# Optimization experiments

Measured on AMD Instinct MI355X. Metric: run time of the kernel, lower is better.

Reference implementation:

```python
import jax, jax.numpy as jnp
import numpy as np

B, S, D, H = 4, 2048, 1024, 16
DH = D // H  # 64
EPS = 1e-5


def setup_inputs() -> dict:
    key = jax.random.key(0)
    ks = jax.random.split(key, 6)
    scale = 0.02
    return {
        "x": jax.random.normal(ks[0], (B, S, D), dtype=jnp.float32),
        "Wq": jax.random.normal(ks[1], (H, D, DH), dtype=jnp.float32) * scale,
        "Wk": jax.random.normal(ks[2], (H, D, DH), dtype=jnp.float32) * scale,
        "Wv": jax.random.normal(ks[3], (H, D, DH), dtype=jnp.float32) * scale,
        "Wo": jax.random.normal(ks[4], (D, D), dtype=jnp.float32) * scale,
        "bo": jnp.zeros((D,), dtype=jnp.float32),
        "gamma": jnp.ones((D,), dtype=jnp.float32),
        "beta": jnp.zeros((D,), dtype=jnp.float32),
    }


def reference(x, Wq, Wk, Wv, Wo, bo, gamma, beta):
    # Per-head projections, stacked across heads: [B,H,S,DH]
    q = jnp.einsum("bsd,hdk->bhsk", x, Wq)
    k = jnp.einsum("bsd,hdk->bhsk", x, Wk)
    v = jnp.einsum("bsd,hdk->bhsk", x, Wv)
    inv_scale = 1.0 / jnp.sqrt(jnp.float32(DH))  # key.size(-1) == head_dim
    scores = jnp.einsum("bhqk,bhsk->bhqs", q, k) * inv_scale  # [B,H,S,S]
    attn = jax.nn.softmax(scores, axis=-1)
    ctx = jnp.einsum("bhqs,bhsk->bhqk", attn, v)  # [B,H,S,DH]
    # concat heads -> [B,S,D]
    concat = jnp.transpose(ctx, (0, 2, 1, 3)).reshape(B, S, D)
    proj = concat @ Wo + bo  # fc_out (Wo stored as [in,out])
    added = proj + x  # residual add
    mu = jnp.mean(added, axis=-1, keepdims=True)
    var = jnp.mean(jnp.square(added - mu), axis=-1, keepdims=True)
    normed = (added - mu) * jax.lax.rsqrt(var + EPS)
    return normed * gamma + beta
```

## Files before the change

### kernel.cpp

```cpp
#include <hip/hip_runtime.h>
#include <hip/hip_bf16.h>
#include <stdint.h>

#define DEV __device__ __forceinline__

typedef short s16x8 __attribute__((ext_vector_type(8)));
typedef float f32x4 __attribute__((ext_vector_type(4)));
typedef int i32x4 __attribute__((ext_vector_type(4)));

DEV void async_load16(const void* g, void* l) {
  __builtin_amdgcn_global_load_lds((void __attribute__((address_space(1)))*)(g),
                                   (void __attribute__((address_space(3)))*)(l),
                                   16, 0, 0);
}

DEV unsigned pack_bf16x2(float a, float b) {
  __hip_bfloat162 h = __float22bfloat162_rn(make_float2(a, b));
  union { __hip_bfloat162 h2; unsigned u; } cv;
  cv.h2 = h;
  return cv.u;
}

__global__ __launch_bounds__(256) void cast_x_kernel(const float* __restrict__ in,
                                                     __hip_bfloat16* __restrict__ out, int n4) {
  int i = blockIdx.x * 256 + threadIdx.x;
  if (i >= n4) return;
  float4 v = ((const float4*)in)[i];
  alignas(8) __hip_bfloat16 t[4] = {__float2bfloat16(v.x), __float2bfloat16(v.y),
                                    __float2bfloat16(v.z), __float2bfloat16(v.w)};
  *(uint2*)(out + (size_t)i * 4) = *(const uint2*)t;
}

__global__ __launch_bounds__(256) void transpose_cast_kernel(const float* __restrict__ src,
                                                             __hip_bfloat16* __restrict__ dst,
                                                             int R, int C, float scale) {
  __shared__ float tile[64][65];
  const int r0 = blockIdx.x * 64, c0 = blockIdx.y * 64, bt = blockIdx.z;
  const int tc = threadIdx.x & 63, tr = threadIdx.x >> 6;
  const float* sp = src + (size_t)bt * R * C;
#pragma unroll
  for (int rr = 0; rr < 64; rr += 4)
    tile[tr + rr][tc] = sp[(size_t)(r0 + tr + rr) * C + c0 + tc];
  __syncthreads();
  __hip_bfloat16* dp = dst + (size_t)bt * R * C;
#pragma unroll
  for (int rr = 0; rr < 64; rr += 4) {
    int cc = tr + rr;
    dp[(size_t)(c0 + cc) * R + r0 + tc] = __float2bfloat16(tile[tc][cc] * scale);
  }
}

__global__ __launch_bounds__(256) void qkv_transpose_kernel(const float* __restrict__ Wq,
                                                            const float* __restrict__ Wk,
                                                            const float* __restrict__ Wv,
                                                            __hip_bfloat16* __restrict__ dst,
                                                            float qscale) {
  __shared__ float tile[64][65];
  const int z = blockIdx.z, which = z >> 4, bt = z & 15;
  const int r0 = blockIdx.x * 64;
  const int tc = threadIdx.x & 63, tr = threadIdx.x >> 6;
  const float* src = (which == 0) ? Wq : (which == 1) ? Wk : Wv;
  const float scale = (which == 0) ? qscale : 1.0f;
  const float* sp = src + (size_t)bt * 1024 * 64;
#pragma unroll
  for (int rr = 0; rr < 64; rr += 4)
    tile[tr + rr][tc] = sp[(size_t)(r0 + tr + rr) * 64 + tc];
  __syncthreads();
  __hip_bfloat16* dp = dst + (size_t)z * 1024 * 64;
#pragma unroll
  for (int rr = 0; rr < 64; rr += 4) {
    int cc = tr + rr;
    dp[(size_t)(cc)*1024 + r0 + tc] = __float2bfloat16(tile[tc][cc] * scale);
  }
}

template <int MODE>
__global__ __launch_bounds__(256) void gemm128(const __hip_bfloat16* __restrict__ A,
                                               const __hip_bfloat16* __restrict__ Bt,
                                               void* __restrict__ out0,
                                               void* __restrict__ out1,
                                               void* __restrict__ out2,
                                               const float* __restrict__ bias,
                                               const float* __restrict__ resid,
                                               int M, int N, int K) {
  __shared__ __hip_bfloat16 As[128 * 32];
  __shared__ __hip_bfloat16 Bs[128 * 32];
  const int tid = threadIdx.x;
  const int lane = tid & 63, w = tid >> 6;
  const int lr = lane & 15, lq = lane >> 4;
  const int wm = w >> 1, wn = w & 1;
  const int m0 = blockIdx.y * 128, n0 = blockIdx.x * 128;

  const f32x4 fz = {0.f, 0.f, 0.f, 0.f};
  f32x4 acc[4][4];
#pragma unroll
  for (int i = 0; i < 4; i++)
#pragma unroll
    for (int j = 0; j < 4; j++) acc[i][j] = fz;

  const int kiters = K >> 5;
  for (int kt = 0; kt < kiters; kt++) {
    __syncthreads();
#pragma unroll
    for (int r = 0; r < 2; r++) {
      const int c = r * 256 + tid;
      const int row = c >> 2, kc = c & 3;
      async_load16((const short*)A + (size_t)(m0 + row) * K + kt * 32 + kc * 8,
                   (char*)As + (r * 256 + (tid & 0xC0)) * 16);
      async_load16((const short*)Bt + (size_t)(n0 + row) * K + kt * 32 + kc * 8,
                   (char*)Bs + (r * 256 + (tid & 0xC0)) * 16);
    }
    __syncthreads();
    const short* Ap = (const short*)As;
    const short* Bp = (const short*)Bs;
    s16x8 av[4], bv[4];
#pragma unroll
    for (int i = 0; i < 4; i++)
      av[i] = *(const s16x8*)(Ap + (wm * 64 + i * 16 + lr) * 32 + lq * 8);
#pragma unroll
    for (int j = 0; j < 4; j++)
      bv[j] = *(const s16x8*)(Bp + (wn * 64 + j * 16 + lr) * 32 + lq * 8);
#pragma unroll
    for (int i = 0; i < 4; i++)
#pragma unroll
      for (int j = 0; j < 4; j++)
        acc[i][j] = __builtin_amdgcn_mfma_f32_16x16x32_bf16(av[i], bv[j], acc[i][j], 0, 0, 0);
  }

  if constexpr (MODE == 0) {
    if (n0 < 2048) {
      __hip_bfloat16* dst01 = (__hip_bfloat16*)((n0 < 1024) ? out0 : out1);
#pragma unroll
      for (int i = 0; i < 4; i++)
#pragma unroll
        for (int j = 0; j < 4; j++)
#pragma unroll
          for (int r = 0; r < 4; r++) {
            const int row = m0 + wm * 64 + i * 16 + lq * 4 + r;
            const int col = n0 + wn * 64 + j * 16 + lr;
            const int bb = row >> 11, s = row & 2047;
            const int colq = col & 1023;
            dst01[((((size_t)bb * 16 + (colq >> 6)) * 2048 + s) << 6) + (col & 63)] =
                __float2bfloat16(acc[i][j][r]);
          }
    } else {
#pragma unroll
      for (int i = 0; i < 4; i++)
#pragma unroll
        for (int j = 0; j < 4; j++) {
          const int row0 = m0 + wm * 64 + i * 16 + lq * 4;
          const int col = (n0 - 2048) + wn * 64 + j * 16 + lr;
          const int bb = row0 >> 11, s0 = row0 & 2047;
          alignas(8) __hip_bfloat16 t4[4] = {
              __float2bfloat16(acc[i][j][0]), __float2bfloat16(acc[i][j][1]),
              __float2bfloat16(acc[i][j][2]), __float2bfloat16(acc[i][j][3])};
          *(uint2*)((__hip_bfloat16*)out2 + (size_t)bb * 2097152 + (size_t)col * 2048 + s0) =
              *(const uint2*)t4;
        }
    }
  } else {
#pragma unroll
    for (int i = 0; i < 4; i++)
#pragma unroll
      for (int j = 0; j < 4; j++)
#pragma unroll
        for (int r = 0; r < 4; r++) {
          const int row = m0 + wm * 64 + i * 16 + lq * 4 + r;
          const int col = n0 + wn * 64 + j * 16 + lr;
          const size_t idx = (size_t)row * 1024 + col;
          ((float*)out0)[idx] = acc[i][j][r] + bias[col] + resid[idx];
        }
  }
}

__global__ __launch_bounds__(256, 4) void flash_kernel(const __hip_bfloat16* __restrict__ Qg,
                                                       const __hip_bfloat16* __restrict__ Kg,
                                                       const __hip_bfloat16* __restrict__ Vtg,
                                                       __hip_bfloat16* __restrict__ Og) {
  __shared__ alignas(16) char smem[32768];
  float* xch = (float*)smem;
  const int tid = threadIdx.x;
  const int lane = tid & 63, w = tid >> 6;
  const int lr = lane & 15, lq = lane >> 4;
  const int qp = w >> 1;
  const int kvh = w & 1;
  const int hb = blockIdx.x, qt = blockIdx.y;
  const int h = hb >> 2, b = hb & 3;
  const size_t bh = (size_t)b * 16 + h;
  const short* Qbase = (const short*)Qg + (bh * 2048 + (size_t)qt * 64) * 64;
  const short* Kbh = (const short*)Kg + bh * 2048 * 64;
  const short* Vbh = (const short*)Vtg + bh * 64 * 2048;

  const int rbase = (lr >> 2) * 8 + (lr & 3);
  const int gk = lr & 7;

  s16x8 qb[2][2];
#pragma unroll
  for (int ntl = 0; ntl < 2; ntl++)
#pragma unroll
    for (int ks = 0; ks < 2; ks++)
      qb[ntl][ks] =
          *(const s16x8*)(Qbase + ((qp * 2 + ntl) * 16 + lr) * 64 + ks * 32 + lq * 8);

  s16x8 vones;
#pragma unroll
  for (int e = 0; e < 8; e++) vones[e] = (short)0x3F80;

  const f32x4 fz = {0.f, 0.f, 0.f, 0.f};
  f32x4 o[2][4];
  f32x4 ol[2];
#pragma unroll
  for (int i = 0; i < 2; i++) {
    ol[i] = fz;
#pragma unroll
    for (int j = 0; j < 4; j++) o[i][j] = fz;
  }

  auto stage = [&](int sel, int kb) {
    char* Kl = smem + sel * 16384;
    char* Vl = Kl + 8192;
    const short* Ksrc = Kbh + kb * 64 * 64;
#pragma unroll
    for (int r = 0; r < 2; r++) {
      int c = r * 256 + tid;
      int row = c >> 3, ck = c & 7;
      int g = (row & 3) | (((row >> 3) & 1) << 2);
      async_load16(Ksrc + row * 64 + (ck ^ g) * 8, Kl + (r * 256 + (tid & 0xC0)) * 16);
    }
#pragma unroll
    for (int r = 0; r < 2; r++) {
      int c = r * 256 + tid;
      int row = c >> 3, ck = c & 7;
      async_load16(Vbh + (size_t)row * 2048 + kb * 64 + ((ck ^ (row & 7))) * 8,
                   Vl + (r * 256 + (tid & 0xC0)) * 16);
    }
  };

  stage(0, 0);
  __syncthreads();

  for (int kb = 0; kb < 32; kb++) {
    const int cur = kb & 1;
    if (kb + 1 < 32) stage(cur ^ 1, kb + 1);

    const short* Kp = (const short*)(smem + cur * 16384);
    const short* Vp = (const short*)(smem + cur * 16384 + 8192);

    union { i32x4 i; s16x8 s; } pa[2];
#pragma unroll
    for (int mt = 0; mt < 2; mt++) {
      const int kvrow = kvh * 32 + mt * 4 + rbase;
      s16x8 kf0 = *(const s16x8*)(Kp + kvrow * 64 + (((0 * 4 + lq) ^ gk)) * 8);
      s16x8 kf1 = *(const s16x8*)(Kp + kvrow * 64 + (((1 * 4 + lq) ^ gk)) * 8);
#pragma unroll
      for (int ntl = 0; ntl < 2; ntl++) {
        f32x4 st = fz;
        st = __builtin_amdgcn_mfma_f32_16x16x32_bf16(kf0, qb[ntl][0], st, 0, 0, 0);
        st = __builtin_amdgcn_mfma_f32_16x16x32_bf16(kf1, qb[ntl][1], st, 0, 0, 0);
        float e0 = __builtin_amdgcn_exp2f(st[0]);
        float e1 = __builtin_amdgcn_exp2f(st[1]);
        float e2 = __builtin_amdgcn_exp2f(st[2]);
        float e3 = __builtin_amdgcn_exp2f(st[3]);
        pa[ntl].i[mt * 2 + 0] = (int)pack_bf16x2(e0, e1);
        pa[ntl].i[mt * 2 + 1] = (int)pack_bf16x2(e2, e3);
      }
    }
    __builtin_amdgcn_s_setprio(1);
#pragma unroll
    for (int ntl = 0; ntl < 2; ntl++)
      ol[ntl] = __builtin_amdgcn_mfma_f32_16x16x32_bf16(pa[ntl].s, vones, ol[ntl], 0, 0, 0);
#pragma unroll
    for (int ndh = 0; ndh < 4; ndh++) {
      int vrow = ndh * 16 + lr;
      s16x8 vb = *(const s16x8*)(Vp + vrow * 64 + (((kvh * 4 + lq) ^ (vrow & 7))) * 8);
#pragma unroll
      for (int ntl = 0; ntl < 2; ntl++)
        o[ntl][ndh] =
            __builtin_amdgcn_mfma_f32_16x16x32_bf16(pa[ntl].s, vb, o[ntl][ndh], 0, 0, 0);
    }
    __builtin_amdgcn_s_setprio(0);

    __syncthreads();
  }

  float* slot = xch + w * 1280;
  if (kvh == 0) {
#pragma unroll
    for (int ndh = 0; ndh < 4; ndh++)
      *(f32x4*)(slot + ndh * 256 + lane * 4) = o[1][ndh];
    *(f32x4*)(slot + 1024 + lane * 4) = ol[1];
  } else {
#pragma unroll
    for (int ndh = 0; ndh < 4; ndh++)
      *(f32x4*)(slot + ndh * 256 + lane * 4) = o[0][ndh];
    *(f32x4*)(slot + 1024 + lane * 4) = ol[0];
  }
  __syncthreads();
  const float* ps = xch + (w ^ 1) * 1280;
  if (kvh == 0) {
#pragma unroll
    for (int ndh = 0; ndh < 4; ndh++)
      o[0][ndh] += *(const f32x4*)(ps + ndh * 256 + lane * 4);
    f32x4 lt = ol[0] + *(const f32x4*)(ps + 1024 + lane * 4);
#pragma unroll
    for (int r = 0; r < 4; r++) {
      float inv = __builtin_amdgcn_rcpf(lt[r]);
      int rowg = qt * 64 + w * 16 + lq * 4 + r;
#pragma unroll
      for (int ndh = 0; ndh < 4; ndh++)
        Og[((size_t)b * 2048 + rowg) * 1024 + h * 64 + ndh * 16 + lr] =
            __float2bfloat16(o[0][ndh][r] * inv);
    }
  } else {
#pragma unroll
    for (int ndh = 0; ndh < 4; ndh++)
      o[1][ndh] += *(const f32x4*)(ps + ndh * 256 + lane * 4);
    f32x4 lt = ol[1] + *(const f32x4*)(ps + 1024 + lane * 4);
#pragma unroll
    for (int r = 0; r < 4; r++) {
      float inv = __builtin_amdgcn_rcpf(lt[r]);
      int rowg = qt * 64 + w * 16 + lq * 4 + r;
#pragma unroll
      for (int ndh = 0; ndh < 4; ndh++)
        Og[((size_t)b * 2048 + rowg) * 1024 + h * 64 + ndh * 16 + lr] =
            __float2bfloat16(o[1][ndh][r] * inv);
    }
  }
}

__global__ __launch_bounds__(256) void ln_kernel(const float* __restrict__ tmp,
                                                 const float* __restrict__ gamma,
                                                 const float* __restrict__ beta,
                                                 float* __restrict__ out) {
  const int row = blockIdx.x, tid = threadIdx.x;
  const int lane = tid & 63, w = tid >> 6;
  const float* rp = tmp + (size_t)row * 1024;
  float4 v = ((const float4*)rp)[tid];
  float s = v.x + v.y + v.z + v.w;
  float ss = v.x * v.x + v.y * v.y + v.z * v.z + v.w * v.w;
#pragma unroll
  for (int off = 32; off >= 1; off >>= 1) {
    s += __shfl_xor(s, off);
    ss += __shfl_xor(ss, off);
  }
  __shared__ float red[8];
  if (lane == 0) {
    red[w] = s;
    red[4 + w] = ss;
  }
  __syncthreads();
  s = red[0] + red[1] + red[2] + red[3];
  ss = red[4] + red[5] + red[6] + red[7];
  const float mu = s * (1.0f / 1024.0f);
  const float var = ss * (1.0f / 1024.0f) - mu * mu;
  const float rstd = rsqrtf(var + 1e-5f);
  float4 g = ((const float4*)gamma)[tid];
  float4 be = ((const float4*)beta)[tid];
  float4 ov;
  ov.x = (v.x - mu) * rstd * g.x + be.x;
  ov.y = (v.y - mu) * rstd * g.y + be.y;
  ov.z = (v.z - mu) * rstd * g.z + be.z;
  ov.w = (v.w - mu) * rstd * g.w + be.w;
  ((float4*)(out + (size_t)row * 1024))[tid] = ov;
}

extern "C" void kernel_launch(void* const* d_in, const int* in_sizes, int n_in,
                              void* d_out, int out_size, void* d_ws, size_t ws_size,
                              hipStream_t stream) {
  (void)in_sizes; (void)n_in; (void)out_size; (void)ws_size;
  const float* x = (const float*)d_in[0];
  const float* Wq = (const float*)d_in[1];
  const float* Wk = (const float*)d_in[2];
  const float* Wv = (const float*)d_in[3];
  const float* Wo = (const float*)d_in[4];
  const float* bo = (const float*)d_in[5];
  const float* gamma = (const float*)d_in[6];
  const float* beta = (const float*)d_in[7];
  float* out = (float*)d_out;
  char* ws = (char*)d_ws;

  __hip_bfloat16* xb = (__hip_bfloat16*)(ws + 0);
  __hip_bfloat16* wqkvT = (__hip_bfloat16*)(ws + 16777216);
  __hip_bfloat16* woT = (__hip_bfloat16*)(ws + 23068672);
  __hip_bfloat16* Q = (__hip_bfloat16*)(ws + 25165824);
  __hip_bfloat16* Kt = (__hip_bfloat16*)(ws + 41943040);
  __hip_bfloat16* Vt = (__hip_bfloat16*)(ws + 58720256);
  __hip_bfloat16* cc = (__hip_bfloat16*)(ws + 75497472);
  float* tmp = (float*)(ws + 25165824);

  cast_x_kernel<<<8192, 256, 0, stream>>>(x, xb, 2097152);
  qkv_transpose_kernel<<<dim3(16, 1, 48), 256, 0, stream>>>(Wq, Wk, Wv, wqkvT,
                                                            0.125f * 1.44269504088896f);
  transpose_cast_kernel<<<dim3(16, 16, 1), 256, 0, stream>>>(Wo, woT, 1024, 1024, 1.0f);

  gemm128<0><<<dim3(24, 64), 256, 0, stream>>>(xb, wqkvT, Q, Kt, Vt, nullptr, nullptr,
                                               8192, 3072, 1024);

  flash_kernel<<<dim3(64, 32), 256, 0, stream>>>(Q, Kt, Vt, cc);

  gemm128<2><<<dim3(8, 64), 256, 0, stream>>>(cc, woT, tmp, nullptr, nullptr, bo, x,
                                              8192, 1024, 1024);
  ln_kernel<<<8192, 256, 0, stream>>>(tmp, gamma, beta, out);
}
```

Before: 307.3 us.

## Load K/V fragments directly from global memory instead of staging through LDS

The flash attention kernel drops its double-buffered async global-to-LDS staging of K and V tiles and per-iteration barriers. Each wave now reads its K and V MFMA fragments straight from global memory into registers, and LDS is kept only for the final cross-wave reduction buffer. The occupancy hint changes from 4 to 3 blocks per CU to allow more registers. This removes LDS traffic and synchronisation but duplicates global/L2 reads across waves and loses the explicit prefetch overlap.

```diff
diff --git a/kernel.cpp b/kernel.cpp
--- a/kernel.cpp
+++ b/kernel.cpp
@@ -173,12 +173,11 @@
   }
 }
 
-__global__ __launch_bounds__(256, 4) void flash_kernel(const __hip_bfloat16* __restrict__ Qg,
+__global__ __launch_bounds__(256, 3) void flash_kernel(const __hip_bfloat16* __restrict__ Qg,
                                                        const __hip_bfloat16* __restrict__ Kg,
                                                        const __hip_bfloat16* __restrict__ Vtg,
                                                        __hip_bfloat16* __restrict__ Og) {
-  __shared__ alignas(16) char smem[32768];
-  float* xch = (float*)smem;
+  __shared__ alignas(16) float xch[4 * 1280];
   const int tid = threadIdx.x;
   const int lane = tid & 63, w = tid >> 6;
   const int lr = lane & 15, lq = lane >> 4;
@@ -192,7 +191,6 @@
   const short* Vbh = (const short*)Vtg + bh * 64 * 2048;
 
   const int rbase = (lr >> 2) * 8 + (lr & 3);
-  const int gk = lr & 7;
 
   s16x8 qb[2][2];
 #pragma unroll
@@ -216,47 +214,31 @@
     for (int j = 0; j < 4; j++) o[i][j] = fz;
   }
 
-  auto stage = [&](int sel, int kb) {
-    char* Kl = smem + sel * 16384;
-    char* Vl = Kl + 8192;
-    const short* Ksrc = Kbh + kb * 64 * 64;
-#pragma unroll
-    for (int r = 0; r < 2; r++) {
-      int c = r * 256 + tid;
-      int row = c >> 3, ck = c & 7;
-      int g = (row & 3) | (((row >> 3) & 1) << 2);
-      async_load16(Ksrc + row * 64 + (ck ^ g) * 8, Kl + (r * 256 + (tid & 0xC0)) * 16);
-    }
-#pragma unroll
-    for (int r = 0; r < 2; r++) {
-      int c = r * 256 + tid;
-      int row = c >> 3, ck = c & 7;
-      async_load16(Vbh + (size_t)row * 2048 + kb * 64 + ((ck ^ (row & 7))) * 8,
-                   Vl + (r * 256 + (tid & 0xC0)) * 16);
-    }
-  };
-
-  stage(0, 0);
-  __syncthreads();
+  const short* Kw = Kbh + (size_t)(kvh * 32 + rbase) * 64 + lq * 8;
+  const short* Vw = Vbh + (size_t)lr * 2048 + kvh * 32 + lq * 8;
 
   for (int kb = 0; kb < 32; kb++) {
-    const int cur = kb & 1;
-    if (kb + 1 < 32) stage(cur ^ 1, kb + 1);
-
-    const short* Kp = (const short*)(smem + cur * 16384);
-    const short* Vp = (const short*)(smem + cur * 16384 + 8192);
+    const short* Kt = Kw + kb * 4096;
+    const short* Vc = Vw + kb * 64;
+    s16x8 kf[2][2];
+#pragma unroll
+    for (int mt = 0; mt < 2; mt++) {
+      kf[mt][0] = *(const s16x8*)(Kt + mt * 256);
+      kf[mt][1] = *(const s16x8*)(Kt + mt * 256 + 32);
+    }
+    s16x8 vb[4];
+#pragma unroll
+    for (int ndh = 0; ndh < 4; ndh++)
+      vb[ndh] = *(const s16x8*)(Vc + ndh * 32768);
 
     union { i32x4 i; s16x8 s; } pa[2];
 #pragma unroll
     for (int mt = 0; mt < 2; mt++) {
-      const int kvrow = kvh * 32 + mt * 4 + rbase;
-      s16x8 kf0 = *(const s16x8*)(Kp + kvrow * 64 + (((0 * 4 + lq) ^ gk)) * 8);
-      s16x8 kf1 = *(const s16x8*)(Kp + kvrow * 64 + (((1 * 4 + lq) ^ gk)) * 8);
 #pragma unroll
       for (int ntl = 0; ntl < 2; ntl++) {
         f32x4 st = fz;
-        st = __builtin_amdgcn_mfma_f32_16x16x32_bf16(kf0, qb[ntl][0], st, 0, 0, 0);
-        st = __builtin_amdgcn_mfma_f32_16x16x32_bf16(kf1, qb[ntl][1], st, 0, 0, 0);
+        st = __builtin_amdgcn_mfma_f32_16x16x32_bf16(kf[mt][0], qb[ntl][0], st, 0, 0, 0);
+        st = __builtin_amdgcn_mfma_f32_16x16x32_bf16(kf[mt][1], qb[ntl][1], st, 0, 0, 0);
         float e0 = __builtin_amdgcn_exp2f(st[0]);
         float e1 = __builtin_amdgcn_exp2f(st[1]);
         float e2 = __builtin_amdgcn_exp2f(st[2]);
@@ -270,17 +252,12 @@
     for (int ntl = 0; ntl < 2; ntl++)
       ol[ntl] = __builtin_amdgcn_mfma_f32_16x16x32_bf16(pa[ntl].s, vones, ol[ntl], 0, 0, 0);
 #pragma unroll
-    for (int ndh = 0; ndh < 4; ndh++) {
-      int vrow = ndh * 16 + lr;
-      s16x8 vb = *(const s16x8*)(Vp + vrow * 64 + (((kvh * 4 + lq) ^ (vrow & 7))) * 8);
+    for (int ndh = 0; ndh < 4; ndh++)
 #pragma unroll
       for (int ntl = 0; ntl < 2; ntl++)
         o[ntl][ndh] =
-            __builtin_amdgcn_mfma_f32_16x16x32_bf16(pa[ntl].s, vb, o[ntl][ndh], 0, 0, 0);
-    }
+            __builtin_amdgcn_mfma_f32_16x16x32_bf16(pa[ntl].s, vb[ndh], o[ntl][ndh], 0, 0, 0);
     __builtin_amdgcn_s_setprio(0);
-
-    __syncthreads();
   }
 
   float* slot = xch + w * 1280;
```

New measurement: 448.7 us. 1.46x slower.
